# Optimization experiments

Measured on AMD Instinct MI355X. Metric: run time of the kernel, lower is better.

The kernel has to match this reference:

```python
import jax, jax.numpy as jnp
import numpy as np

DIM = 256
NUM_HEADS = 8
HEAD_DIM = DIM // NUM_HEADS


def setup_inputs() -> dict:
    key = jax.random.key(0)
    k1, k2, k3, k4 = jax.random.split(key, 4)
    b, n = 4, 2048
    x = jax.random.normal(k1, (b, n, DIM), dtype=jnp.float32)
    # Linear weights with fan-in scaling (matches nn.Linear init magnitude,
    # keeps exp(qk) numerically sane since the original has no max-subtraction).
    Wqkv = jax.random.normal(k2, (DIM, 3 * DIM), dtype=jnp.float32) * (DIM ** -0.5)
    Wout = jax.random.normal(k3, (DIM, DIM), dtype=jnp.float32) * (DIM ** -0.5)
    bout = jax.random.normal(k4, (DIM,), dtype=jnp.float32) * 0.01
    return {"x": x, "Wqkv": Wqkv, "Wout": Wout, "bout": bout}


def reference(x, Wqkv, Wout, bout):
    b, n, d = x.shape
    h, hd = NUM_HEADS, HEAD_DIM
    scale = hd ** -0.5
    qkv = x @ Wqkv  # [b, n, 3d]
    q, k, v = jnp.split(qkv, 3, axis=-1)
    # [b, h, n, hd]
    q = q.reshape(b, n, h, hd).transpose(0, 2, 1, 3) * scale
    k = k.reshape(b, n, h, hd).transpose(0, 2, 1, 3)
    v = v.reshape(b, n, h, hd).transpose(0, 2, 1, 3)
    # Original KeOps path: unnormalized exp (no max-subtraction), separate
    # numerator / denominator reductions, eps in denominator.
    scores = jnp.einsum('bhnd,bhmd->bhnm', q, k)  # [b, h, n, n]
    e = jnp.exp(scores)
    denom = jnp.sum(e, axis=-1, keepdims=True)          # [b, h, n, 1]
    numer = jnp.einsum('bhnm,bhmd->bhnd', e, v)         # [b, h, n, hd]
    out = numer / (denom + 1e-6)
    out = out.transpose(0, 2, 1, 3).reshape(b, n, d)
    return out @ Wout + bout
```

## Files before the change

### kernel.cpp

```cpp
#include <hip/hip_runtime.h>

#define DIM 256
#define NHEADS 8
#define HDIM 32

typedef _Float16 half8_t __attribute__((ext_vector_type(8)));
typedef float float4_t __attribute__((ext_vector_type(4)));

__device__ __forceinline__ void gload_lds16(const void* g, void* l) {
    __builtin_amdgcn_global_load_lds((const __attribute__((address_space(1))) void*)g,
                                     (__attribute__((address_space(3))) void*)l,
                                     16, 0, 0);
}

__global__ __launch_bounds__(256) void prep(const float* __restrict__ x,
                                            const float* __restrict__ Wqkv,
                                            const float* __restrict__ Wout,
                                            _Float16* __restrict__ xh,
                                            _Float16* __restrict__ WqT,
                                            _Float16* __restrict__ WoT) {
    __shared__ float ts[32][33];
    const int bid = blockIdx.x, t = threadIdx.x;
    if (bid < 1024) {
        size_t idx = (size_t)bid * 2048 + (size_t)t * 8;
        float tmp[8];
        *reinterpret_cast<float4*>(tmp)     = *reinterpret_cast<const float4*>(x + idx);
        *reinterpret_cast<float4*>(tmp + 4) = *reinterpret_cast<const float4*>(x + idx + 4);
        half8_t h;
        #pragma unroll
        for (int j = 0; j < 8; ++j) h[j] = (_Float16)tmp[j];
        *reinterpret_cast<half8_t*>(xh + idx) = h;
    } else {
        const float* src; _Float16* dst; int K, N, kb, nb;
        if (bid < 1024 + 192) { int b2 = bid - 1024; src = Wqkv; dst = WqT; K = 256; N = 768; nb = b2 % 24; kb = b2 / 24; }
        else                  { int b3 = bid - 1216; src = Wout; dst = WoT; K = 256; N = 256; nb = b3 % 8;  kb = b3 / 8; }
        const int tx = t & 31, ty = t >> 5;
        #pragma unroll
        for (int i = 0; i < 4; ++i) {
            int k = kb * 32 + ty + i * 8;
            ts[ty + i * 8][tx] = src[(size_t)k * N + nb * 32 + tx];
        }
        __syncthreads();
        #pragma unroll
        for (int i = 0; i < 4; ++i) {
            int nl = ty + i * 8;
            dst[(size_t)(nb * 32 + nl) * K + kb * 32 + tx] = (_Float16)ts[tx][nl];
        }
    }
}

template <bool OUT_HALF>
__global__ __launch_bounds__(256) void gemm_h(const _Float16* __restrict__ A,
                                              const _Float16* __restrict__ BT,
                                              const float* __restrict__ bias,
                                              void* __restrict__ Cv,
                                              int M, int N, int K) {
    __shared__ alignas(16) _Float16 As[128 * 32];
    __shared__ alignas(16) _Float16 Bs[128 * 32];
    const int t = threadIdx.x, lane = t & 63, wave = t >> 6;
    const int l16 = lane & 15, quad = lane >> 4;
    const int m0 = blockIdx.y * 128, n0 = blockIdx.x * 128;
    const int wr = (wave >> 1) * 64, wc = (wave & 1) * 64;
    float4_t acc[4][4];
    #pragma unroll
    for (int i = 0; i < 4; ++i)
        #pragma unroll
        for (int j = 0; j < 4; ++j) acc[i][j] = (float4_t){0.f, 0.f, 0.f, 0.f};

    const int srow = lane >> 2;
    const int scol = (lane & 3) * 8;

    for (int k0 = 0; k0 < K; k0 += 32) {
        #pragma unroll
        for (int i = 0; i < 2; ++i) {
            int chunk = i * 4 + wave;
            int r = chunk * 16 + srow;
            gload_lds16(A  + (size_t)(m0 + r) * K + k0 + scol, As + chunk * 512);
            gload_lds16(BT + (size_t)(n0 + r) * K + k0 + scol, Bs + chunk * 512);
        }
        __syncthreads();
        half8_t af[4], bf[4];
        #pragma unroll
        for (int i = 0; i < 4; ++i)
            af[i] = *reinterpret_cast<const half8_t*>(As + (wr + i * 16 + l16) * 32 + quad * 8);
        #pragma unroll
        for (int j = 0; j < 4; ++j)
            bf[j] = *reinterpret_cast<const half8_t*>(Bs + (wc + j * 16 + l16) * 32 + quad * 8);
        #pragma unroll
        for (int i = 0; i < 4; ++i)
            #pragma unroll
            for (int j = 0; j < 4; ++j)
                acc[i][j] = __builtin_amdgcn_mfma_f32_16x16x32_f16(af[i], bf[j], acc[i][j], 0, 0, 0);
        __syncthreads();
    }

    float bv[4] = {0.f, 0.f, 0.f, 0.f};
    if (bias != nullptr) {
        #pragma unroll
        for (int j = 0; j < 4; ++j) bv[j] = bias[n0 + wc + j * 16 + l16];
    }
    #pragma unroll
    for (int i = 0; i < 4; ++i)
        #pragma unroll
        for (int r = 0; r < 4; ++r) {
            int row = m0 + wr + i * 16 + quad * 4 + r;
            #pragma unroll
            for (int j = 0; j < 4; ++j) {
                int col = n0 + wc + j * 16 + l16;
                float v = acc[i][j][r] + bv[j];
                if (OUT_HALF) ((_Float16*)Cv)[(size_t)row * N + col] = (_Float16)v;
                else          ((float*)Cv)[(size_t)row * N + col] = v;
            }
        }
}

__global__ __launch_bounds__(256) void attn_mfma(const _Float16* __restrict__ qkv,
                                                 _Float16* __restrict__ outp, int n) {
    __shared__ alignas(16) _Float16 ks[64 * 32];
    __shared__ alignas(16) _Float16 vsT[32 * 64];
    __shared__ alignas(16) _Float16 es[64 * 64];
    const int nqt = n / 64;
    const int bid = blockIdx.x;
    const int qt = bid % nqt;
    const int h  = (bid / nqt) % NHEADS;
    const int b  = bid / (nqt * NHEADS);
    const int t  = threadIdx.x, lane = t & 63, wave = t >> 6;
    const int l16 = lane & 15, quad = lane >> 4;
    const float scale = 0.17677669529663687f;
    const _Float16* base = qkv + (size_t)b * n * (3 * DIM);
    const int q0 = qt * 64 + wave * 16;

    half8_t qf = *reinterpret_cast<const half8_t*>(
        base + (size_t)(q0 + l16) * (3 * DIM) + h * HDIM + quad * 8);

    float4_t numer0 = {0.f, 0.f, 0.f, 0.f};
    float4_t numer1 = {0.f, 0.f, 0.f, 0.f};
    float dsum[4] = {0.f, 0.f, 0.f, 0.f};

    const int kk = t >> 2;
    const int d0 = (t & 3) * 8;

    for (int k0 = 0; k0 < n; k0 += 64) {
        gload_lds16(base + (size_t)(k0 + wave * 16 + (lane >> 2)) * (3 * DIM)
                        + DIM + h * HDIM + (lane & 3) * 8,
                    ks + wave * 512);
        half8_t vt = *reinterpret_cast<const half8_t*>(
            base + (size_t)(k0 + kk) * (3 * DIM) + 2 * DIM + h * HDIM + d0);
        #pragma unroll
        for (int j = 0; j < 8; ++j) {
            int hd = d0 + j;
            int swz = (hd + 2 * (hd >> 3)) & 7;
            int phys8 = (kk >> 3) ^ swz;
            vsT[hd * 64 + phys8 * 8 + (kk & 7)] = vt[j];
        }
        __syncthreads();

        float4_t sf[4];
        #pragma unroll
        for (int kb = 0; kb < 4; ++kb) {
            half8_t kf = *reinterpret_cast<const half8_t*>(ks + (kb * 16 + l16) * 32 + quad * 8);
            float4_t z = {0.f, 0.f, 0.f, 0.f};
            sf[kb] = __builtin_amdgcn_mfma_f32_16x16x32_f16(qf, kf, z, 0, 0, 0);
        }

        #pragma unroll
        for (int kb = 0; kb < 4; ++kb)
            #pragma unroll
            for (int r = 0; r < 4; ++r) {
                float e = __expf(sf[kb][r] * scale);
                dsum[r] += e;
                int qrow = wave * 16 + quad * 4 + r;
                int col  = kb * 16 + l16;
                int swz  = ((qrow >> 2) & 3) * 2;
                int phys8 = (col >> 3) ^ swz;
                es[qrow * 64 + phys8 * 8 + (col & 7)] = (_Float16)e;
            }

        #pragma unroll
        for (int s = 0; s < 2; ++s) {
            int qrow = wave * 16 + l16;
            int swzq = ((qrow >> 2) & 3) * 2;
            half8_t ef = *reinterpret_cast<const half8_t*>(
                es + qrow * 64 + (((s * 4 + quad) ^ swzq) * 8));
            int hd0 = l16, hd1 = 16 + l16;
            int swv0 = (hd0 + 2 * (hd0 >> 3)) & 7;
            int swv1 = (hd1 + 2 * (hd1 >> 3)) & 7;
            half8_t vf0 = *reinterpret_cast<const half8_t*>(
                vsT + hd0 * 64 + (((s * 4 + quad) ^ swv0) * 8));
            half8_t vf1 = *reinterpret_cast<const half8_t*>(
                vsT + hd1 * 64 + (((s * 4 + quad) ^ swv1) * 8));
            numer0 = __builtin_amdgcn_mfma_f32_16x16x32_f16(ef, vf0, numer0, 0, 0, 0);
            numer1 = __builtin_amdgcn_mfma_f32_16x16x32_f16(ef, vf1, numer1, 0, 0, 0);
        }
        __syncthreads();
    }

    #pragma unroll
    for (int off = 1; off < 16; off <<= 1)
        #pragma unroll
        for (int r = 0; r < 4; ++r) dsum[r] += __shfl_xor(dsum[r], off, 16);

    _Float16* ob = outp + ((size_t)b * n + q0) * DIM + h * HDIM;
    #pragma unroll
    for (int r = 0; r < 4; ++r) {
        int row = quad * 4 + r;
        float rcp = 1.0f / (dsum[r] + 1e-6f);
        ob[(size_t)row * DIM + l16]      = (_Float16)(numer0[r] * rcp);
        ob[(size_t)row * DIM + 16 + l16] = (_Float16)(numer1[r] * rcp);
    }
}

extern "C" void kernel_launch(void* const* d_in, const int* in_sizes, int n_in,
                              void* d_out, int out_size, void* d_ws, size_t ws_size,
                              hipStream_t stream) {
    const float* x    = (const float*)d_in[0];
    const float* Wqkv = (const float*)d_in[1];
    const float* Wout = (const float*)d_in[2];
    const float* bout = (const float*)d_in[3];
    float* out = (float*)d_out;
    const int B = 4, N = 2048;
    const int M = B * N;

    _Float16* xh    = (_Float16*)d_ws;
    _Float16* WqT   = xh + (size_t)M * DIM;
    _Float16* WoT   = WqT + 768 * 256;
    _Float16* qkvh  = WoT + 256 * 256;
    _Float16* attnh = qkvh + (size_t)M * 3 * DIM;

    hipLaunchKernelGGL(prep, dim3(1280), dim3(256), 0, stream, x, Wqkv, Wout, xh, WqT, WoT);
    hipLaunchKernelGGL((gemm_h<true>), dim3(6, 64), dim3(256), 0, stream,
                       xh, WqT, (const float*)nullptr, (void*)qkvh, M, 3 * DIM, DIM);
    hipLaunchKernelGGL(attn_mfma, dim3(B * NHEADS * (N / 64)), dim3(256), 0, stream,
                       qkvh, attnh, N);
    hipLaunchKernelGGL((gemm_h<false>), dim3(2, 64), dim3(256), 0, stream,
                       attnh, WoT, bout, (void*)out, M, DIM, DIM);
}
```

Measured before the change: 141.7 us.

## Rewrite GEMMs as register-direct tiles and attention with pre-transposed V

The QKV GEMM now writes V directly in a per-head transposed layout, so the attention kernel can load V fragments straight from global memory. The LDS staging and block barriers for K and V are gone. The attention kernel computes S^T with K as the A operand and uses 32 queries per wave, keeping only a small per-wave LDS buffer to reshuffle exp scores. Both GEMMs switch to 64x64 tiles that load operands directly into registers without LDS. This trades LDS reuse for more global and L2 traffic and a larger grid.

Measured after the change: 164.5 us. 16.1% more time.

```diff
diff --git a/kernel.cpp b/kernel.cpp
--- a/kernel.cpp
+++ b/kernel.cpp
@@ -5,13 +5,8 @@
 #define HDIM 32
 
 typedef _Float16 half8_t __attribute__((ext_vector_type(8)));
+typedef _Float16 half4_t __attribute__((ext_vector_type(4)));
 typedef float float4_t __attribute__((ext_vector_type(4)));
-
-__device__ __forceinline__ void gload_lds16(const void* g, void* l) {
-    __builtin_amdgcn_global_load_lds((const __attribute__((address_space(1))) void*)g,
-                                     (__attribute__((address_space(3))) void*)l,
-                                     16, 0, 0);
-}
 
 __global__ __launch_bounds__(256) void prep(const float* __restrict__ x,
                                             const float* __restrict__ Wqkv,
@@ -49,165 +44,172 @@
     }
 }
 
-template <bool OUT_HALF>
-__global__ __launch_bounds__(256) void gemm_h(const _Float16* __restrict__ A,
+template <bool OUT_HALF, bool VSPLIT>
+__global__ __launch_bounds__(256) void gemm_g(const _Float16* __restrict__ A,
                                               const _Float16* __restrict__ BT,
                                               const float* __restrict__ bias,
                                               void* __restrict__ Cv,
-                                              int M, int N, int K) {
-    __shared__ alignas(16) _Float16 As[128 * 32];
-    __shared__ alignas(16) _Float16 Bs[128 * 32];
+                                              _Float16* __restrict__ VT,
+                                              int M, int N, int K, int ldc) {
+    const int t = threadIdx.x, lane = t & 63;
+    const int wave = t >> 6;
+    const int l16 = lane & 15, quad = lane >> 4;
+    const int m0 = blockIdx.y * 64, n0 = blockIdx.x * 64;
+    const int wr = (wave >> 1) * 32, wc = (wave & 1) * 32;
+
+    float4_t acc[2][2];
+    #pragma unroll
+    for (int i = 0; i < 2; ++i)
+        #pragma unroll
+        for (int j = 0; j < 2; ++j) acc[i][j] = (float4_t){0.f, 0.f, 0.f, 0.f};
+
+    const _Float16* ap0 = A  + (size_t)(m0 + wr + l16) * K + quad * 8;
+    const _Float16* ap1 = ap0 + (size_t)16 * K;
+    const _Float16* bp0 = BT + (size_t)(n0 + wc + l16) * K + quad * 8;
+    const _Float16* bp1 = bp0 + (size_t)16 * K;
+
+    #pragma unroll 4
+    for (int k0 = 0; k0 < K; k0 += 32) {
+        half8_t a0 = *reinterpret_cast<const half8_t*>(ap0 + k0);
+        half8_t a1 = *reinterpret_cast<const half8_t*>(ap1 + k0);
+        half8_t b0 = *reinterpret_cast<const half8_t*>(bp0 + k0);
+        half8_t b1 = *reinterpret_cast<const half8_t*>(bp1 + k0);
+        acc[0][0] = __builtin_amdgcn_mfma_f32_16x16x32_f16(a0, b0, acc[0][0], 0, 0, 0);
+        acc[0][1] = __builtin_amdgcn_mfma_f32_16x16x32_f16(a0, b1, acc[0][1], 0, 0, 0);
+        acc[1][0] = __builtin_amdgcn_mfma_f32_16x16x32_f16(a1, b0, acc[1][0], 0, 0, 0);
+        acc[1][1] = __builtin_amdgcn_mfma_f32_16x16x32_f16(a1, b1, acc[1][1], 0, 0, 0);
+    }
+
+    if (VSPLIT && n0 >= 512) {
+        const int bb = m0 >> 11;
+        const int tok0 = (m0 & 2047) + wr;
+        #pragma unroll
+        for (int i = 0; i < 2; ++i)
+            #pragma unroll
+            for (int j = 0; j < 2; ++j) {
+                int vcol = n0 + wc + j * 16 + l16 - 512;
+                int hh = vcol >> 5, d = vcol & 31;
+                half4_t p;
+                #pragma unroll
+                for (int r = 0; r < 4; ++r) p[r] = (_Float16)acc[i][j][r];
+                *reinterpret_cast<half4_t*>(
+                    VT + ((size_t)(bb * NHEADS + hh) * HDIM + d) * 2048
+                       + tok0 + i * 16 + quad * 4) = p;
+            }
+    } else {
+        #pragma unroll
+        for (int i = 0; i < 2; ++i)
+            #pragma unroll
+            for (int r = 0; r < 4; ++r) {
+                int row = m0 + wr + i * 16 + quad * 4 + r;
+                #pragma unroll
+                for (int j = 0; j < 2; ++j) {
+                    int col = n0 + wc + j * 16 + l16;
+                    float v = acc[i][j][r] + (bias ? bias[col] : 0.f);
+                    if (OUT_HALF) ((_Float16*)Cv)[(size_t)row * ldc + col] = (_Float16)v;
+                    else          ((float*)Cv)[(size_t)row * ldc + col] = v;
+                }
+            }
+    }
+}
+
+__global__ __launch_bounds__(256) void attn_v3(const _Float16* __restrict__ qkh,
+                                               const _Float16* __restrict__ VT,
+                                               _Float16* __restrict__ outp) {
+    __shared__ alignas(16) _Float16 es[4][32][40];
+    const int bid = blockIdx.x;
+    const int qb = bid & 15, bh = bid >> 4;
+    const int b = bh >> 3, h = bh & 7;
     const int t = threadIdx.x, lane = t & 63, wave = t >> 6;
     const int l16 = lane & 15, quad = lane >> 4;
-    const int m0 = blockIdx.y * 128, n0 = blockIdx.x * 128;
-    const int wr = (wave >> 1) * 64, wc = (wave & 1) * 64;
-    float4_t acc[4][4];
-    #pragma unroll
-    for (int i = 0; i < 4; ++i)
-        #pragma unroll
-        for (int j = 0; j < 4; ++j) acc[i][j] = (float4_t){0.f, 0.f, 0.f, 0.f};
-
-    const int srow = lane >> 2;
-    const int scol = (lane & 3) * 8;
-
-    for (int k0 = 0; k0 < K; k0 += 32) {
-        #pragma unroll
-        for (int i = 0; i < 2; ++i) {
-            int chunk = i * 4 + wave;
-            int r = chunk * 16 + srow;
-            gload_lds16(A  + (size_t)(m0 + r) * K + k0 + scol, As + chunk * 512);
-            gload_lds16(BT + (size_t)(n0 + r) * K + k0 + scol, Bs + chunk * 512);
-        }
-        __syncthreads();
-        half8_t af[4], bf[4];
-        #pragma unroll
-        for (int i = 0; i < 4; ++i)
-            af[i] = *reinterpret_cast<const half8_t*>(As + (wr + i * 16 + l16) * 32 + quad * 8);
-        #pragma unroll
-        for (int j = 0; j < 4; ++j)
-            bf[j] = *reinterpret_cast<const half8_t*>(Bs + (wc + j * 16 + l16) * 32 + quad * 8);
-        #pragma unroll
-        for (int i = 0; i < 4; ++i)
-            #pragma unroll
-            for (int j = 0; j < 4; ++j)
-                acc[i][j] = __builtin_amdgcn_mfma_f32_16x16x32_f16(af[i], bf[j], acc[i][j], 0, 0, 0);
-        __syncthreads();
-    }
-
-    float bv[4] = {0.f, 0.f, 0.f, 0.f};
-    if (bias != nullptr) {
-        #pragma unroll
-        for (int j = 0; j < 4; ++j) bv[j] = bias[n0 + wc + j * 16 + l16];
-    }
-    #pragma unroll
-    for (int i = 0; i < 4; ++i)
+    const float scale = 0.17677669529663687f;
+    const int bN = b * 2048;
+    const int q0w = qb * 128 + wave * 32;
+
+    const _Float16* qrow = qkh + (size_t)(bN + q0w + l16) * 512 + h * HDIM + quad * 8;
+    half8_t qf0 = *reinterpret_cast<const half8_t*>(qrow);
+    half8_t qf1 = *reinterpret_cast<const half8_t*>(qrow + (size_t)16 * 512);
+
+    const _Float16* kbase = qkh + (size_t)(bN + l16) * 512 + 256 + h * HDIM + quad * 8;
+    const _Float16* vbase = VT + (size_t)bh * HDIM * 2048 + (size_t)l16 * 2048 + quad * 8;
+
+    float4_t num[2][2];
+    #pragma unroll
+    for (int g = 0; g < 2; ++g)
+        #pragma unroll
+        for (int dt = 0; dt < 2; ++dt) num[g][dt] = (float4_t){0.f, 0.f, 0.f, 0.f};
+    float ds[2] = {0.f, 0.f};
+    _Float16* esw = &es[wave][0][0];
+    const float4_t z = {0.f, 0.f, 0.f, 0.f};
+
+    for (int k0 = 0; k0 < 2048; k0 += 64) {
+        const _Float16* kp = kbase + (size_t)k0 * 512;
+        half8_t kf0 = *reinterpret_cast<const half8_t*>(kp);
+        half8_t kf1 = *reinterpret_cast<const half8_t*>(kp + (size_t)16 * 512);
+        half8_t kf2 = *reinterpret_cast<const half8_t*>(kp + (size_t)32 * 512);
+        half8_t kf3 = *reinterpret_cast<const half8_t*>(kp + (size_t)48 * 512);
+
+        float4_t st[4][2];
+        st[0][0] = __builtin_amdgcn_mfma_f32_16x16x32_f16(kf0, qf0, z, 0, 0, 0);
+        st[0][1] = __builtin_amdgcn_mfma_f32_16x16x32_f16(kf0, qf1, z, 0, 0, 0);
+        st[1][0] = __builtin_amdgcn_mfma_f32_16x16x32_f16(kf1, qf0, z, 0, 0, 0);
+        st[1][1] = __builtin_amdgcn_mfma_f32_16x16x32_f16(kf1, qf1, z, 0, 0, 0);
+        st[2][0] = __builtin_amdgcn_mfma_f32_16x16x32_f16(kf2, qf0, z, 0, 0, 0);
+        st[2][1] = __builtin_amdgcn_mfma_f32_16x16x32_f16(kf2, qf1, z, 0, 0, 0);
+        st[3][0] = __builtin_amdgcn_mfma_f32_16x16x32_f16(kf3, qf0, z, 0, 0, 0);
+        st[3][1] = __builtin_amdgcn_mfma_f32_16x16x32_f16(kf3, qf1, z, 0, 0, 0);
+
+        half4_t ep[4][2];
+        #pragma unroll
+        for (int kb = 0; kb < 4; ++kb)
+            #pragma unroll
+            for (int g = 0; g < 2; ++g)
+                #pragma unroll
+                for (int r = 0; r < 4; ++r) {
+                    float e = __expf(st[kb][g][r] * scale);
+                    ds[g] += e;
+                    ep[kb][g][r] = (_Float16)e;
+                }
+
+        #pragma unroll
+        for (int s = 0; s < 2; ++s) {
+            #pragma unroll
+            for (int tt = 0; tt < 2; ++tt)
+                #pragma unroll
+                for (int g = 0; g < 2; ++g)
+                    *reinterpret_cast<half4_t*>(
+                        esw + (g * 16 + l16) * 40 + tt * 16 + quad * 4) = ep[s * 2 + tt][g];
+
+            half8_t ef0 = *reinterpret_cast<const half8_t*>(esw + l16 * 40 + quad * 8);
+            half8_t ef1 = *reinterpret_cast<const half8_t*>(esw + (16 + l16) * 40 + quad * 8);
+
+            const _Float16* vp = vbase + k0 + s * 32;
+            half8_t vf0 = *reinterpret_cast<const half8_t*>(vp);
+            half8_t vf1 = *reinterpret_cast<const half8_t*>(vp + (size_t)16 * 2048);
+
+            num[0][0] = __builtin_amdgcn_mfma_f32_16x16x32_f16(ef0, vf0, num[0][0], 0, 0, 0);
+            num[0][1] = __builtin_amdgcn_mfma_f32_16x16x32_f16(ef0, vf1, num[0][1], 0, 0, 0);
+            num[1][0] = __builtin_amdgcn_mfma_f32_16x16x32_f16(ef1, vf0, num[1][0], 0, 0, 0);
+            num[1][1] = __builtin_amdgcn_mfma_f32_16x16x32_f16(ef1, vf1, num[1][1], 0, 0, 0);
+        }
+    }
+
+    #pragma unroll
+    for (int g = 0; g < 2; ++g) {
+        ds[g] += __shfl_xor(ds[g], 16, 64);
+        ds[g] += __shfl_xor(ds[g], 32, 64);
+    }
+
+    _Float16* ob = outp + (size_t)(bN + q0w) * DIM + h * HDIM;
+    #pragma unroll
+    for (int g = 0; g < 2; ++g)
         #pragma unroll
         for (int r = 0; r < 4; ++r) {
-            int row = m0 + wr + i * 16 + quad * 4 + r;
-            #pragma unroll
-            for (int j = 0; j < 4; ++j) {
-                int col = n0 + wc + j * 16 + l16;
-                float v = acc[i][j][r] + bv[j];
-                if (OUT_HALF) ((_Float16*)Cv)[(size_t)row * N + col] = (_Float16)v;
-                else          ((float*)Cv)[(size_t)row * N + col] = v;
-            }
-        }
-}
-
-__global__ __launch_bounds__(256) void attn_mfma(const _Float16* __restrict__ qkv,
-                                                 _Float16* __restrict__ outp, int n) {
-    __shared__ alignas(16) _Float16 ks[64 * 32];
-    __shared__ alignas(16) _Float16 vsT[32 * 64];
-    __shared__ alignas(16) _Float16 es[64 * 64];
-    const int nqt = n / 64;
-    const int bid = blockIdx.x;
-    const int qt = bid % nqt;
-    const int h  = (bid / nqt) % NHEADS;
-    const int b  = bid / (nqt * NHEADS);
-    const int t  = threadIdx.x, lane = t & 63, wave = t >> 6;
-    const int l16 = lane & 15, quad = lane >> 4;
-    const float scale = 0.17677669529663687f;
-    const _Float16* base = qkv + (size_t)b * n * (3 * DIM);
-    const int q0 = qt * 64 + wave * 16;
-
-    half8_t qf = *reinterpret_cast<const half8_t*>(
-        base + (size_t)(q0 + l16) * (3 * DIM) + h * HDIM + quad * 8);
-
-    float4_t numer0 = {0.f, 0.f, 0.f, 0.f};
-    float4_t numer1 = {0.f, 0.f, 0.f, 0.f};
-    float dsum[4] = {0.f, 0.f, 0.f, 0.f};
-
-    const int kk = t >> 2;
-    const int d0 = (t & 3) * 8;
-
-    for (int k0 = 0; k0 < n; k0 += 64) {
-        gload_lds16(base + (size_t)(k0 + wave * 16 + (lane >> 2)) * (3 * DIM)
-                        + DIM + h * HDIM + (lane & 3) * 8,
-                    ks + wave * 512);
-        half8_t vt = *reinterpret_cast<const half8_t*>(
-            base + (size_t)(k0 + kk) * (3 * DIM) + 2 * DIM + h * HDIM + d0);
-        #pragma unroll
-        for (int j = 0; j < 8; ++j) {
-            int hd = d0 + j;
-            int swz = (hd + 2 * (hd >> 3)) & 7;
-            int phys8 = (kk >> 3) ^ swz;
-            vsT[hd * 64 + phys8 * 8 + (kk & 7)] = vt[j];
-        }
-        __syncthreads();
-
-        float4_t sf[4];
-        #pragma unroll
-        for (int kb = 0; kb < 4; ++kb) {
-            half8_t kf = *reinterpret_cast<const half8_t*>(ks + (kb * 16 + l16) * 32 + quad * 8);
-            float4_t z = {0.f, 0.f, 0.f, 0.f};
-            sf[kb] = __builtin_amdgcn_mfma_f32_16x16x32_f16(qf, kf, z, 0, 0, 0);
-        }
-
-        #pragma unroll
-        for (int kb = 0; kb < 4; ++kb)
-            #pragma unroll
-            for (int r = 0; r < 4; ++r) {
-                float e = __expf(sf[kb][r] * scale);
-                dsum[r] += e;
-                int qrow = wave * 16 + quad * 4 + r;
-                int col  = kb * 16 + l16;
-                int swz  = ((qrow >> 2) & 3) * 2;
-                int phys8 = (col >> 3) ^ swz;
-                es[qrow * 64 + phys8 * 8 + (col & 7)] = (_Float16)e;
-            }
-
-        #pragma unroll
-        for (int s = 0; s < 2; ++s) {
-            int qrow = wave * 16 + l16;
-            int swzq = ((qrow >> 2) & 3) * 2;
-            half8_t ef = *reinterpret_cast<const half8_t*>(
-                es + qrow * 64 + (((s * 4 + quad) ^ swzq) * 8));
-            int hd0 = l16, hd1 = 16 + l16;
-            int swv0 = (hd0 + 2 * (hd0 >> 3)) & 7;
-            int swv1 = (hd1 + 2 * (hd1 >> 3)) & 7;
-            half8_t vf0 = *reinterpret_cast<const half8_t*>(
-                vsT + hd0 * 64 + (((s * 4 + quad) ^ swv0) * 8));
-            half8_t vf1 = *reinterpret_cast<const half8_t*>(
-                vsT + hd1 * 64 + (((s * 4 + quad) ^ swv1) * 8));
-            numer0 = __builtin_amdgcn_mfma_f32_16x16x32_f16(ef, vf0, numer0, 0, 0, 0);
-            numer1 = __builtin_amdgcn_mfma_f32_16x16x32_f16(ef, vf1, numer1, 0, 0, 0);
-        }
-        __syncthreads();
-    }
-
-    #pragma unroll
-    for (int off = 1; off < 16; off <<= 1)
-        #pragma unroll
-        for (int r = 0; r < 4; ++r) dsum[r] += __shfl_xor(dsum[r], off, 16);
-
-    _Float16* ob = outp + ((size_t)b * n + q0) * DIM + h * HDIM;
-    #pragma unroll
-    for (int r = 0; r < 4; ++r) {
-        int row = quad * 4 + r;
-        float rcp = 1.0f / (dsum[r] + 1e-6f);
-        ob[(size_t)row * DIM + l16]      = (_Float16)(numer0[r] * rcp);
-        ob[(size_t)row * DIM + 16 + l16] = (_Float16)(numer1[r] * rcp);
-    }
+            float rcp = 1.0f / (__shfl(ds[g], quad * 4 + r, 64) + 1e-6f);
+            size_t ro = (size_t)(g * 16 + quad * 4 + r) * DIM;
+            ob[ro + l16]      = (_Float16)(num[g][0][r] * rcp);
+            ob[ro + 16 + l16] = (_Float16)(num[g][1][r] * rcp);
+        }
 }
 
 extern "C" void kernel_launch(void* const* d_in, const int* in_sizes, int n_in,
@@ -218,20 +220,19 @@
     const float* Wout = (const float*)d_in[2];
     const float* bout = (const float*)d_in[3];
     float* out = (float*)d_out;
-    const int B = 4, N = 2048;
-    const int M = B * N;
+    const int M = 8192;
 
     _Float16* xh    = (_Float16*)d_ws;
     _Float16* WqT   = xh + (size_t)M * DIM;
     _Float16* WoT   = WqT + 768 * 256;
-    _Float16* qkvh  = WoT + 256 * 256;
-    _Float16* attnh = qkvh + (size_t)M * 3 * DIM;
+    _Float16* qkh   = WoT + 256 * 256;
+    _Float16* vt    = qkh + (size_t)M * 512;
+    _Float16* attnh = vt + (size_t)32 * HDIM * 2048;
 
     hipLaunchKernelGGL(prep, dim3(1280), dim3(256), 0, stream, x, Wqkv, Wout, xh, WqT, WoT);
-    hipLaunchKernelGGL((gemm_h<true>), dim3(6, 64), dim3(256), 0, stream,
-                       xh, WqT, (const float*)nullptr, (void*)qkvh, M, 3 * DIM, DIM);
-    hipLaunchKernelGGL(attn_mfma, dim3(B * NHEADS * (N / 64)), dim3(256), 0, stream,
-                       qkvh, attnh, N);
-    hipLaunchKernelGGL((gemm_h<false>), dim3(2, 64), dim3(256), 0, stream,
-                       attnh, WoT, bout, (void*)out, M, DIM, DIM);
-}
+    hipLaunchKernelGGL((gemm_g<true, true>), dim3(12, 128), dim3(256), 0, stream,
+                       xh, WqT, (const float*)nullptr, (void*)qkh, vt, M, 768, DIM, 512);
+    hipLaunchKernelGGL(attn_v3, dim3(512), dim3(256), 0, stream, qkh, vt, attnh);
+    hipLaunchKernelGGL((gemm_g<false, false>), dim3(4, 128), dim3(256), 0, stream,
+                       attnh, WoT, bout, (void*)out, (_Float16*)nullptr, M, DIM, DIM, DIM);
+}
```
